# Optimization experiments

Measured on AMD Instinct MI355X. Metric: run time of the kernel, lower is better.

The kernel has to match this reference:

```python
import jax, jax.numpy as jnp
import numpy as np

N = 100000        # nodes
E = 3200000       # edges (avg degree 32)
IN, HID, OUT = 512, 256, 64
K = 10
ALPHA = 0.1


def setup_inputs() -> dict:
    key = jax.random.key(0)
    k1, k2, k3, k4 = jax.random.split(key, 4)
    x = jax.random.normal(k1, (N, IN), dtype=jnp.float32)
    edge_index = jax.random.randint(k2, (2, E), 0, N, dtype=jnp.int64)
    W1 = jax.random.normal(k3, (IN, HID), dtype=jnp.float32) * (1.0 / np.sqrt(IN))
    b1 = jnp.zeros((HID,), dtype=jnp.float32)
    W2 = jax.random.normal(k4, (HID, OUT), dtype=jnp.float32) * (1.0 / np.sqrt(HID))
    b2 = jnp.zeros((OUT,), dtype=jnp.float32)
    return {"x": x, "edge_index": edge_index, "W1": W1, "b1": b1, "W2": W2, "b2": b2}


def reference(x, edge_index, W1, b1, W2, b2):
    # MLP head: Linear -> ReLU -> Linear
    h = jax.nn.relu(x @ W1 + b1)
    h = h @ W2 + b2                                   # [N, OUT]

    # gcn_norm with self-loops: D^-1/2 (A + I) D^-1/2
    src = jnp.concatenate([edge_index[0], jnp.arange(N, dtype=edge_index.dtype)])
    dst = jnp.concatenate([edge_index[1], jnp.arange(N, dtype=edge_index.dtype)])
    deg = jax.ops.segment_sum(jnp.ones_like(src, dtype=h.dtype), dst, num_segments=N)
    dinv = jnp.where(deg > 0, jax.lax.rsqrt(deg), 0.0)
    norm = dinv[src] * dinv[dst]                      # [E+N]

    h0 = h

    def step(h, _):
        msg = h[src] * norm[:, None]                  # gather + edge scale
        agg = jax.ops.segment_sum(msg, dst, num_segments=N)  # scatter-add
        h = (1.0 - ALPHA) * agg + ALPHA * h0          # teleport
        return h, None

    h, _ = jax.lax.scan(step, h, None, length=K)
    return h
```

## Files before the change

### kernel.cpp

```cpp
#include <hip/hip_runtime.h>
#include <hip/hip_bf16.h>
#include <hip/hip_fp16.h>


typedef __bf16 bf16x8 __attribute__((ext_vector_type(8)));
typedef float f32x4 __attribute__((ext_vector_type(4)));

static constexpr int IN = 512, HID = 256, OUT = 64;
static constexpr int LDT = 40;

static __device__ __forceinline__ ushort f2bf(float f) {
  __hip_bfloat16 b = __float2bfloat16(f);
  return *reinterpret_cast<ushort*>(&b);
}
static __device__ __forceinline__ float bf2f(ushort u) {
  unsigned int x = ((unsigned int)u) << 16;
  return __uint_as_float(x);
}
static __device__ __forceinline__ float h15f(unsigned int u) {
  ushort hb = (ushort)(u & 0x7FFFu);
  __half h = *reinterpret_cast<__half*>(&hb);
  return __half2float(h);
}

__global__ void transpose_f32_bf16(const float* __restrict__ in, ushort* __restrict__ out,
                                   int K, int C) {
  int idx = blockIdx.x * 256 + threadIdx.x;
  if (idx < K * C) {
    int n = idx / K, k = idx % K;
    out[idx] = f2bf(in[k * C + n]);
  }
}

__global__ __launch_bounds__(256) void gemm1(const float* __restrict__ X,
                                             const ushort* __restrict__ W1T,
                                             const float* __restrict__ b1,
                                             ushort* __restrict__ h1, int M) {
  __shared__ __align__(16) ushort As[128 * LDT];
  __shared__ __align__(16) ushort Bs[128 * LDT];
  const int tid = threadIdx.x;
  const int m0 = blockIdx.x * 128;
  const int n0 = blockIdx.y * 128;
  const int lane = tid & 63, w = tid >> 6;
  const int wr = w >> 1, wc = w & 1;
  const int lm = lane & 15, lq = lane >> 4;
  const int cB = tid & 3, rB = tid >> 2;
  const int cA = tid & 7, rA = tid >> 3;

  f32x4 acc[4][4] = {};

  for (int k0 = 0; k0 < IN; k0 += 32) {
#pragma unroll
    for (int rr = 0; rr < 4; ++rr) {
      int m = rA + rr * 32;
      int gm = m0 + m; gm = gm < M ? gm : M - 1;
      float4 f = *reinterpret_cast<const float4*>(&X[(size_t)gm * IN + k0 + cA * 4]);
      ushort4 cv;
      cv.x = f2bf(f.x); cv.y = f2bf(f.y); cv.z = f2bf(f.z); cv.w = f2bf(f.w);
      *reinterpret_cast<ushort4*>(&As[m * LDT + cA * 4]) = cv;
    }
#pragma unroll
    for (int rr = 0; rr < 2; ++rr) {
      int n = rB + rr * 64;
      *reinterpret_cast<int4*>(&Bs[n * LDT + cB * 8]) =
          *reinterpret_cast<const int4*>(&W1T[(size_t)(n0 + n) * IN + k0 + cB * 8]);
    }
    __syncthreads();
    bf16x8 af[4], bq[4];
#pragma unroll
    for (int mi = 0; mi < 4; ++mi)
      af[mi] = *reinterpret_cast<const bf16x8*>(&As[(wr * 64 + mi * 16 + lm) * LDT + lq * 8]);
#pragma unroll
    for (int ni = 0; ni < 4; ++ni)
      bq[ni] = *reinterpret_cast<const bf16x8*>(&Bs[(wc * 64 + ni * 16 + lm) * LDT + lq * 8]);
#pragma unroll
    for (int mi = 0; mi < 4; ++mi)
#pragma unroll
      for (int ni = 0; ni < 4; ++ni)
        acc[mi][ni] = __builtin_amdgcn_mfma_f32_16x16x32_bf16(af[mi], bq[ni], acc[mi][ni], 0, 0, 0);
    __syncthreads();
  }

#pragma unroll
  for (int ni = 0; ni < 4; ++ni) {
    int col = n0 + wc * 64 + ni * 16 + lm;
    float bias = b1[col];
#pragma unroll
    for (int mi = 0; mi < 4; ++mi) {
#pragma unroll
      for (int rg = 0; rg < 4; ++rg) {
        int row = m0 + wr * 64 + mi * 16 + lq * 4 + rg;
        if (row < M) {
          float v = acc[mi][ni][rg] + bias;
          v = v > 0.f ? v : 0.f;
          h1[(size_t)row * HID + col] = f2bf(v);
        }
      }
    }
  }
}

__global__ __launch_bounds__(256) void gemm2(const ushort* __restrict__ h1,
                                             const ushort* __restrict__ W2T,
                                             const float* __restrict__ b2,
                                             float* __restrict__ H0f,
                                             ushort* __restrict__ H0b, int M) {
  __shared__ __align__(16) ushort As[128 * LDT];
  __shared__ __align__(16) ushort Bs[64 * LDT];
  const int tid = threadIdx.x;
  const int m0 = blockIdx.x * 128;
  const int lane = tid & 63, w = tid >> 6;
  const int lm = lane & 15, lq = lane >> 4;
  const int c = tid & 3, r = tid >> 2;

  f32x4 acc[2][4] = {};

  for (int k0 = 0; k0 < HID; k0 += 32) {
#pragma unroll
    for (int rr = 0; rr < 2; ++rr) {
      int m = r + rr * 64;
      int gm = m0 + m; gm = gm < M ? gm : M - 1;
      *reinterpret_cast<int4*>(&As[m * LDT + c * 8]) =
          *reinterpret_cast<const int4*>(&h1[(size_t)gm * HID + k0 + c * 8]);
    }
    *reinterpret_cast<int4*>(&Bs[r * LDT + c * 8]) =
        *reinterpret_cast<const int4*>(&W2T[(size_t)r * HID + k0 + c * 8]);
    __syncthreads();
    bf16x8 af[2], bq[4];
#pragma unroll
    for (int mi = 0; mi < 2; ++mi)
      af[mi] = *reinterpret_cast<const bf16x8*>(&As[(w * 32 + mi * 16 + lm) * LDT + lq * 8]);
#pragma unroll
    for (int ni = 0; ni < 4; ++ni)
      bq[ni] = *reinterpret_cast<const bf16x8*>(&Bs[(ni * 16 + lm) * LDT + lq * 8]);
#pragma unroll
    for (int mi = 0; mi < 2; ++mi)
#pragma unroll
      for (int ni = 0; ni < 4; ++ni)
        acc[mi][ni] = __builtin_amdgcn_mfma_f32_16x16x32_bf16(af[mi], bq[ni], acc[mi][ni], 0, 0, 0);
    __syncthreads();
  }

#pragma unroll
  for (int ni = 0; ni < 4; ++ni) {
    int col = ni * 16 + lm;
    float bias = b2[col];
#pragma unroll
    for (int mi = 0; mi < 2; ++mi) {
#pragma unroll
      for (int rg = 0; rg < 4; ++rg) {
        int row = m0 + w * 32 + mi * 16 + lq * 4 + rg;
        if (row < M) {
          float v = acc[mi][ni][rg] + bias;
          H0f[(size_t)row * OUT + col] = v;
          H0b[(size_t)row * OUT + col] = f2bf(v);
        }
      }
    }
  }
}

__global__ void count_deg(const int* __restrict__ ei, int* __restrict__ cnt, int E) {
  int e = blockIdx.x * 256 + threadIdx.x;
  if (e < E) atomicAdd(&cnt[ei[E + e]], 1);
}

__global__ void calc_dinv(const int* __restrict__ cnt, float* __restrict__ dinv, int n) {
  int v = blockIdx.x * 256 + threadIdx.x;
  if (v < n) dinv[v] = rsqrtf((float)cnt[v] + 1.0f);
}

__global__ __launch_bounds__(1024) void scan_kernel(const int* __restrict__ cnt,
                                                    int* __restrict__ offs,
                                                    int* __restrict__ cursor, int n) {
  __shared__ int wsum[16];
  __shared__ int woff[16];
  __shared__ int carry_s;
  const int tid = threadIdx.x;
  const int lane = tid & 63, wid = tid >> 6;
  if (tid == 0) carry_s = 0;
  __syncthreads();
  for (int base = 0; base < n; base += 4096) {
    int i0 = base + tid * 4;
    int x[4];
#pragma unroll
    for (int j = 0; j < 4; ++j) x[j] = (i0 + j < n) ? cnt[i0 + j] : 0;
    int tsum = x[0] + x[1] + x[2] + x[3];
    int val = tsum;
#pragma unroll
    for (int d = 1; d < 64; d <<= 1) {
      int t = __shfl_up(val, d, 64);
      if (lane >= d) val += t;
    }
    if (lane == 63) wsum[wid] = val;
    __syncthreads();
    if (wid == 0) {
      int s = (lane < 16) ? wsum[lane] : 0;
      int sv = s;
#pragma unroll
      for (int d = 1; d < 16; d <<= 1) {
        int t = __shfl_up(sv, d, 64);
        if (lane >= d) sv += t;
      }
      if (lane < 16) woff[lane] = sv - s;
    }
    __syncthreads();
    int excl = carry_s + woff[wid] + (val - tsum);
#pragma unroll
    for (int j = 0; j < 4; ++j) {
      if (i0 + j < n) { offs[i0 + j] = excl; cursor[i0 + j] = excl; }
      excl += x[j];
    }
    __syncthreads();
    if (tid == 1023) carry_s = excl;
    __syncthreads();
  }
  if (tid == 0) offs[n] = carry_s;
}

__global__ void fill_csr(const int* __restrict__ ei, int* __restrict__ cursor,
                         const float* __restrict__ dinv, unsigned int* __restrict__ csr,
                         int E) {
  int e = blockIdx.x * 256 + threadIdx.x;
  if (e < E) {
    int s = ei[e], d = ei[E + e];
    int p = atomicAdd(&cursor[d], 1);
    float w = dinv[s] * dinv[d];
    __half hw = __float2half(w);
    unsigned int hb = *reinterpret_cast<ushort*>(&hw);
    csr[p] = (((unsigned int)s) << 15) | hb;
  }
}

template <bool WRITE_BF>
__global__ __launch_bounds__(256) void prop_step(const float* __restrict__ hinf,
                                                 const ushort* __restrict__ hinb,
                                                 float* __restrict__ houtf,
                                                 ushort* __restrict__ houtb,
                                                 const float* __restrict__ h0,
                                                 const int* __restrict__ offs,
                                                 const unsigned int* __restrict__ csr,
                                                 const float* __restrict__ dinv, int n) {
  int gw = (blockIdx.x * 256 + threadIdx.x) >> 6;
  int lane = threadIdx.x & 63;
  if (gw >= n) return;
  float dv = dinv[gw];
  float a[8];
  a[0] = hinf[(size_t)gw * OUT + lane] * dv * dv;
#pragma unroll
  for (int k = 1; k < 8; ++k) a[k] = 0.f;
  int e0 = offs[gw], e1 = offs[gw + 1];
  for (int base = e0; base < e1; base += 64) {
    int rem = e1 - base;
    unsigned int my = (lane < rem) ? csr[base + lane] : 0u;
    int cnt = rem < 64 ? rem : 64;
    int cnt16 = (cnt + 15) & ~15;
    for (int j = 0; j < cnt16; j += 16) {
      unsigned int u[16];
#pragma unroll
      for (int k = 0; k < 16; ++k) u[k] = (unsigned int)__shfl((int)my, j + k);
      float v[16];
#pragma unroll
      for (int k = 0; k < 16; ++k)
        v[k] = bf2f(hinb[(size_t)(u[k] >> 15) * OUT + lane]);
#pragma unroll
      for (int k = 0; k < 16; ++k) a[k & 7] = fmaf(h15f(u[k]), v[k], a[k & 7]);
    }
  }
  float acc = ((a[0] + a[1]) + (a[2] + a[3])) + ((a[4] + a[5]) + (a[6] + a[7]));
  float o = 0.9f * acc + 0.1f * h0[(size_t)gw * OUT + lane];
  houtf[(size_t)gw * OUT + lane] = o;
  if (WRITE_BF) houtb[(size_t)gw * OUT + lane] = f2bf(o);
}

extern "C" void kernel_launch(void* const* d_in, const int* in_sizes, int n_in,
                              void* d_out, int out_size, void* d_ws, size_t ws_size,
                              hipStream_t stream) {
  const float* X  = (const float*)d_in[0];
  const int*   EI = (const int*)d_in[1];
  const float* W1 = (const float*)d_in[2];
  const float* b1 = (const float*)d_in[3];
  const float* W2 = (const float*)d_in[4];
  const float* b2 = (const float*)d_in[5];
  float* out = (float*)d_out;

  const int N = in_sizes[0] / IN;
  const int E = in_sizes[1] / 2;

  char* ws = (char*)d_ws;
  size_t o = 0;
  auto alloc = [&](size_t b) {
    char* p = ws + o;
    o = (o + b + 255) & ~(size_t)255;
    return p;
  };
  float*  H0f  = (float*)alloc((size_t)N * OUT * 4);
  ushort* H0b  = (ushort*)alloc((size_t)N * OUT * 2);
  float*  hAf  = (float*)alloc((size_t)N * OUT * 4);
  ushort* hAb  = (ushort*)alloc((size_t)N * OUT * 2);
  float*  hBf  = (float*)alloc((size_t)N * OUT * 4);
  ushort* hBb  = (ushort*)alloc((size_t)N * OUT * 2);
  ushort* h1   = (ushort*)alloc((size_t)N * HID * 2);
  ushort* W1T  = (ushort*)alloc((size_t)IN * HID * 2);
  ushort* W2T  = (ushort*)alloc((size_t)HID * OUT * 2);
  int*    cnt  = (int*)alloc((size_t)N * 4);
  int*    offs = (int*)alloc((size_t)(N + 1) * 4);
  int*    curs = (int*)alloc((size_t)N * 4);
  float*  dinv = (float*)alloc((size_t)N * 4);
  unsigned int* csr = (unsigned int*)alloc((size_t)E * 4);
  (void)ws_size; (void)n_in; (void)out_size;

  transpose_f32_bf16<<<(IN * HID + 255) / 256, 256, 0, stream>>>(W1, W1T, IN, HID);
  transpose_f32_bf16<<<(HID * OUT + 255) / 256, 256, 0, stream>>>(W2, W2T, HID, OUT);

  gemm1<<<dim3((N + 127) / 128, HID / 128), 256, 0, stream>>>(X, W1T, b1, h1, N);
  gemm2<<<(N + 127) / 128, 256, 0, stream>>>(h1, W2T, b2, H0f, H0b, N);

  hipMemsetAsync(cnt, 0, (size_t)N * 4, stream);
  count_deg<<<(E + 255) / 256, 256, 0, stream>>>(EI, cnt, E);
  calc_dinv<<<(N + 255) / 256, 256, 0, stream>>>(cnt, dinv, N);
  scan_kernel<<<1, 1024, 0, stream>>>(cnt, offs, curs, N);
  fill_csr<<<(E + 255) / 256, 256, 0, stream>>>(EI, curs, dinv, csr, E);

  const int pgrid = (N * OUT + 255) / 256;
  prop_step<true><<<pgrid, 256, 0, stream>>>(H0f, H0b, hAf, hAb, H0f, offs, csr, dinv, N);
  for (int i = 0; i < 4; ++i) {
    prop_step<true><<<pgrid, 256, 0, stream>>>(hAf, hAb, hBf, hBb, H0f, offs, csr, dinv, N);
    prop_step<true><<<pgrid, 256, 0, stream>>>(hBf, hBb, hAf, hAb, H0f, offs, csr, dinv, N);
  }
  prop_step<false><<<pgrid, 256, 0, stream>>>(hAf, hAb, out, nullptr, H0f, offs, csr, dinv, N);
}
```

Baseline: 1.386 ms.

## Two-pass bucketed CSR build and paired bf16 gather in propagation

CSR construction now first bins edges by destination range (512-node buckets) using shared-memory staging, then scatters each bucket into CSR with atomics confined to a small node range. This is meant to improve locality of the scattered atomic writes. The propagation kernel now has each half-wavefront handle alternate edges and load two bf16 columns per 32-bit word, combining the halves with a cross-lane shuffle. The degree scan processes 8 elements per thread. The change adds an 8-byte-per-edge intermediate buffer and extra kernel launches.

```diff
diff --git a/kernel.cpp b/kernel.cpp
--- a/kernel.cpp
+++ b/kernel.cpp
@@ -8,14 +8,18 @@
 
 static constexpr int IN = 512, HID = 256, OUT = 64;
 static constexpr int LDT = 40;
+static constexpr int BSH = 9;
+static constexpr int BINC = 24;
 
 static __device__ __forceinline__ ushort f2bf(float f) {
   __hip_bfloat16 b = __float2bfloat16(f);
   return *reinterpret_cast<ushort*>(&b);
 }
-static __device__ __forceinline__ float bf2f(ushort u) {
-  unsigned int x = ((unsigned int)u) << 16;
-  return __uint_as_float(x);
+static __device__ __forceinline__ float bf2f_lo(unsigned int v) {
+  return __uint_as_float(v << 16);
+}
+static __device__ __forceinline__ float bf2f_hi(unsigned int v) {
+  return __uint_as_float(v & 0xFFFF0000u);
 }
 static __device__ __forceinline__ float h15f(unsigned int u) {
   ushort hb = (ushort)(u & 0x7FFFu);
@@ -160,14 +164,52 @@
   }
 }
 
-__global__ void count_deg(const int* __restrict__ ei, int* __restrict__ cnt, int E) {
-  int e = blockIdx.x * 256 + threadIdx.x;
-  if (e < E) atomicAdd(&cnt[ei[E + e]], 1);
+__global__ __launch_bounds__(256) void deg_bucket(const int* __restrict__ ei,
+                                                  int* __restrict__ cnt,
+                                                  int* __restrict__ bcnt, int E) {
+  __shared__ int lb[256];
+  int t = threadIdx.x;
+  lb[t] = 0;
+  __syncthreads();
+  int e = blockIdx.x * 1024 + t;
+#pragma unroll
+  for (int k = 0; k < 4; ++k) {
+    if (e < E) {
+      int d = ei[E + e];
+      atomicAdd(&cnt[d], 1);
+      atomicAdd(&lb[d >> BSH], 1);
+    }
+    e += 256;
+  }
+  __syncthreads();
+  if (lb[t]) atomicAdd(&bcnt[t], lb[t]);
 }
 
 __global__ void calc_dinv(const int* __restrict__ cnt, float* __restrict__ dinv, int n) {
   int v = blockIdx.x * 256 + threadIdx.x;
   if (v < n) dinv[v] = rsqrtf((float)cnt[v] + 1.0f);
+}
+
+__global__ __launch_bounds__(256) void bucket_scan(const int* __restrict__ bcnt,
+                                                   int* __restrict__ boff,
+                                                   int* __restrict__ bcur) {
+  __shared__ int ws[4];
+  int t = threadIdx.x, lane = t & 63, wid = t >> 6;
+  int x = bcnt[t];
+  int v = x;
+#pragma unroll
+  for (int d = 1; d < 64; d <<= 1) {
+    int tt = __shfl_up(v, d, 64);
+    if (lane >= d) v += tt;
+  }
+  if (lane == 63) ws[wid] = v;
+  __syncthreads();
+  int off = 0;
+  for (int i = 0; i < wid; ++i) off += ws[i];
+  int excl = off + v - x;
+  boff[t] = excl;
+  bcur[t] = excl;
+  if (t == 255) boff[256] = excl + x;
 }
 
 __global__ __launch_bounds__(1024) void scan_kernel(const int* __restrict__ cnt,
@@ -180,12 +222,14 @@
   const int lane = tid & 63, wid = tid >> 6;
   if (tid == 0) carry_s = 0;
   __syncthreads();
-  for (int base = 0; base < n; base += 4096) {
-    int i0 = base + tid * 4;
-    int x[4];
-#pragma unroll
-    for (int j = 0; j < 4; ++j) x[j] = (i0 + j < n) ? cnt[i0 + j] : 0;
-    int tsum = x[0] + x[1] + x[2] + x[3];
+  for (int base = 0; base < n; base += 8192) {
+    int i0 = base + tid * 8;
+    int x[8];
+#pragma unroll
+    for (int j = 0; j < 8; ++j) x[j] = (i0 + j < n) ? cnt[i0 + j] : 0;
+    int tsum = 0;
+#pragma unroll
+    for (int j = 0; j < 8; ++j) tsum += x[j];
     int val = tsum;
 #pragma unroll
     for (int d = 1; d < 64; d <<= 1) {
@@ -207,7 +251,7 @@
     __syncthreads();
     int excl = carry_s + woff[wid] + (val - tsum);
 #pragma unroll
-    for (int j = 0; j < 4; ++j) {
+    for (int j = 0; j < 8; ++j) {
       if (i0 + j < n) { offs[i0 + j] = excl; cursor[i0 + j] = excl; }
       excl += x[j];
     }
@@ -218,17 +262,57 @@
   if (tid == 0) offs[n] = carry_s;
 }
 
-__global__ void fill_csr(const int* __restrict__ ei, int* __restrict__ cursor,
-                         const float* __restrict__ dinv, unsigned int* __restrict__ csr,
-                         int E) {
-  int e = blockIdx.x * 256 + threadIdx.x;
-  if (e < E) {
-    int s = ei[e], d = ei[E + e];
-    int p = atomicAdd(&cursor[d], 1);
-    float w = dinv[s] * dinv[d];
-    __half hw = __float2half(w);
-    unsigned int hb = *reinterpret_cast<ushort*>(&hw);
-    csr[p] = (((unsigned int)s) << 15) | hb;
+__global__ __launch_bounds__(256) void fill_bins(const int* __restrict__ ei,
+                                                 const float* __restrict__ dinv,
+                                                 int* __restrict__ bcur,
+                                                 int2* __restrict__ bed, int E) {
+  __shared__ int2 buf[256][BINC];
+  __shared__ int lbc[256];
+  const int t = threadIdx.x;
+  const int base = blockIdx.x * 2048;
+  lbc[t] = 0;
+  __syncthreads();
+#pragma unroll
+  for (int k = 0; k < 8; ++k) {
+    int e = base + k * 256 + t;
+    if (e < E) {
+      int s = ei[e], d = ei[E + e];
+      float w = dinv[s] * dinv[d];
+      __half hw = __float2half(w);
+      unsigned int packed = (((unsigned int)s) << 15) | *reinterpret_cast<ushort*>(&hw);
+      int b = d >> BSH;
+      int slot = atomicAdd(&lbc[b], 1);
+      if (slot < BINC) {
+        buf[b][slot] = make_int2(d, (int)packed);
+      } else {
+        int p = atomicAdd(&bcur[b], 1);
+        bed[p] = make_int2(d, (int)packed);
+      }
+    }
+  }
+  __syncthreads();
+  const int lane = t & 63, wid = t >> 6;
+  for (int b = wid; b < 256; b += 4) {
+    int c = lbc[b];
+    if (c > BINC) c = BINC;
+    if (c == 0) continue;
+    int gbase;
+    if (lane == 0) gbase = atomicAdd(&bcur[b], c);
+    gbase = __shfl(gbase, 0);
+    if (lane < c) bed[gbase + lane] = buf[b][lane];
+  }
+}
+
+__global__ __launch_bounds__(256) void csr_scatter(const int2* __restrict__ bed,
+                                                   const int* __restrict__ boff,
+                                                   int* __restrict__ curs,
+                                                   unsigned int* __restrict__ csr) {
+  int b = blockIdx.x;
+  int s = boff[b], e = boff[b + 1];
+  for (int i = s + threadIdx.x; i < e; i += 256) {
+    int2 r = bed[i];
+    int p = atomicAdd(&curs[r.x], 1);
+    csr[p] = (unsigned int)r.y;
   }
 }
 
@@ -241,14 +325,14 @@
                                                  const int* __restrict__ offs,
                                                  const unsigned int* __restrict__ csr,
                                                  const float* __restrict__ dinv, int n) {
-  int gw = (blockIdx.x * 256 + threadIdx.x) >> 6;
-  int lane = threadIdx.x & 63;
+  const int gw = (blockIdx.x * 256 + threadIdx.x) >> 6;
+  const int lane = threadIdx.x & 63;
   if (gw >= n) return;
-  float dv = dinv[gw];
-  float a[8];
-  a[0] = hinf[(size_t)gw * OUT + lane] * dv * dv;
-#pragma unroll
-  for (int k = 1; k < 8; ++k) a[k] = 0.f;
+  const int half = lane >> 5, col = lane & 31;
+  const unsigned int* hin32 = reinterpret_cast<const unsigned int*>(hinb);
+
+  float ax[4] = {0.f, 0.f, 0.f, 0.f};
+  float ay[4] = {0.f, 0.f, 0.f, 0.f};
   int e0 = offs[gw], e1 = offs[gw + 1];
   for (int base = e0; base < e1; base += 64) {
     int rem = e1 - base;
@@ -256,21 +340,39 @@
     int cnt = rem < 64 ? rem : 64;
     int cnt16 = (cnt + 15) & ~15;
     for (int j = 0; j < cnt16; j += 16) {
-      unsigned int u[16];
-#pragma unroll
-      for (int k = 0; k < 16; ++k) u[k] = (unsigned int)__shfl((int)my, j + k);
-      float v[16];
-#pragma unroll
-      for (int k = 0; k < 16; ++k)
-        v[k] = bf2f(hinb[(size_t)(u[k] >> 15) * OUT + lane]);
-#pragma unroll
-      for (int k = 0; k < 16; ++k) a[k & 7] = fmaf(h15f(u[k]), v[k], a[k & 7]);
-    }
-  }
-  float acc = ((a[0] + a[1]) + (a[2] + a[3])) + ((a[4] + a[5]) + (a[6] + a[7]));
-  float o = 0.9f * acc + 0.1f * h0[(size_t)gw * OUT + lane];
-  houtf[(size_t)gw * OUT + lane] = o;
-  if (WRITE_BF) houtb[(size_t)gw * OUT + lane] = f2bf(o);
+      unsigned int u[8];
+#pragma unroll
+      for (int p = 0; p < 8; ++p)
+        u[p] = (unsigned int)__shfl((int)my, j + 2 * p + half);
+      unsigned int v[8];
+#pragma unroll
+      for (int p = 0; p < 8; ++p)
+        v[p] = hin32[(size_t)(u[p] >> 15) * 32 + col];
+#pragma unroll
+      for (int p = 0; p < 8; ++p) {
+        float w = h15f(u[p]);
+        ax[p & 3] = fmaf(w, bf2f_lo(v[p]), ax[p & 3]);
+        ay[p & 3] = fmaf(w, bf2f_hi(v[p]), ay[p & 3]);
+      }
+    }
+  }
+  float tx = (ax[0] + ax[1]) + (ax[2] + ax[3]);
+  float ty = (ay[0] + ay[1]) + (ay[2] + ay[3]);
+  tx += __shfl_xor(tx, 32);
+  ty += __shfl_xor(ty, 32);
+
+  float dv = dinv[gw];
+  float2 sv = *reinterpret_cast<const float2*>(&hinf[(size_t)gw * OUT + 2 * col]);
+  float2 hv = *reinterpret_cast<const float2*>(&h0[(size_t)gw * OUT + 2 * col]);
+  float ox = 0.9f * (tx + sv.x * dv * dv) + 0.1f * hv.x;
+  float oy = 0.9f * (ty + sv.y * dv * dv) + 0.1f * hv.y;
+  if (lane < 32) {
+    *reinterpret_cast<float2*>(&houtf[(size_t)gw * OUT + 2 * col]) = make_float2(ox, oy);
+    if (WRITE_BF) {
+      unsigned int pk = (unsigned int)f2bf(ox) | ((unsigned int)f2bf(oy) << 16);
+      reinterpret_cast<unsigned int*>(houtb)[(size_t)gw * 32 + col] = pk;
+    }
+  }
 }
 
 extern "C" void kernel_launch(void* const* d_in, const int* in_sizes, int n_in,
@@ -307,6 +409,10 @@
   int*    offs = (int*)alloc((size_t)(N + 1) * 4);
   int*    curs = (int*)alloc((size_t)N * 4);
   float*  dinv = (float*)alloc((size_t)N * 4);
+  int*    bcnt = (int*)alloc(256 * 4);
+  int*    boff = (int*)alloc(257 * 4);
+  int*    bcur = (int*)alloc(256 * 4);
+  int2*   bed  = (int2*)alloc((size_t)E * 8);
   unsigned int* csr = (unsigned int*)alloc((size_t)E * 4);
   (void)ws_size; (void)n_in; (void)out_size;
 
@@ -317,10 +423,13 @@
   gemm2<<<(N + 127) / 128, 256, 0, stream>>>(h1, W2T, b2, H0f, H0b, N);
 
   hipMemsetAsync(cnt, 0, (size_t)N * 4, stream);
-  count_deg<<<(E + 255) / 256, 256, 0, stream>>>(EI, cnt, E);
+  hipMemsetAsync(bcnt, 0, 256 * 4, stream);
+  deg_bucket<<<(E + 1023) / 1024, 256, 0, stream>>>(EI, cnt, bcnt, E);
   calc_dinv<<<(N + 255) / 256, 256, 0, stream>>>(cnt, dinv, N);
+  bucket_scan<<<1, 256, 0, stream>>>(bcnt, boff, bcur);
   scan_kernel<<<1, 1024, 0, stream>>>(cnt, offs, curs, N);
-  fill_csr<<<(E + 255) / 256, 256, 0, stream>>>(EI, curs, dinv, csr, E);
+  fill_bins<<<(E + 2047) / 2048, 256, 0, stream>>>(EI, dinv, bcur, bed, E);
+  csr_scatter<<<256, 256, 0, stream>>>(bed, boff, curs, csr);
 
   const int pgrid = (N * OUT + 255) / 256;
   prop_step<true><<<pgrid, 256, 0, stream>>>(H0f, H0b, hAf, hAb, H0f, offs, csr, dinv, N);
```

Result: slower. 2.274 ms (+64.0%).
